# Performance work log

Measured on AMD Instinct MI355X. Metric: run time of the kernel, lower is better.

## Reference

```python
import jax, jax.numpy as jnp
import numpy as np

NUM_HEADS = 12
PER_HEAD_DIM = 64
EMBED_DIM = NUM_HEADS * PER_HEAD_DIM
MAX_LEN = 1024  # max_position_embeddings - 1


def setup_inputs() -> dict:
    key = jax.random.key(0)
    k1, k2, k3 = jax.random.split(key, 3)
    pre_proj_emb = jax.random.normal(k1, (8, MAX_LEN, EMBED_DIM), dtype=jnp.float32)
    # trunc_normal_(mean=0, std=1, a=0, b=1) ~ values in [0,1); uniform is a faithful stand-in for random init
    toeplitz_psfs = jax.random.uniform(k2, (NUM_HEADS, 2 * MAX_LEN - 1, PER_HEAD_DIM), dtype=jnp.float32)
    proj_w = jax.random.normal(k3, (EMBED_DIM, EMBED_DIM), dtype=jnp.float32) * (1.0 / np.sqrt(EMBED_DIM))
    proj_b = jnp.zeros((EMBED_DIM,), dtype=jnp.float32)
    return {"pre_proj_emb": pre_proj_emb, "toeplitz_psfs": toeplitz_psfs, "proj_w": proj_w, "proj_b": proj_b}


def reference(pre_proj_emb, toeplitz_psfs, proj_w, proj_b):
    B, L, D = pre_proj_emb.shape
    H, dh = NUM_HEADS, PER_HEAD_DIM
    # pad sequence to 2L-1 and split heads: [B, 2L-1, H, dh] -> [B, H, 2L-1, dh]
    padded = jnp.pad(pre_proj_emb, ((0, 0), (0, L - 1), (0, 0)))
    padded = padded.reshape(B, 2 * L - 1, H, dh).transpose(0, 2, 1, 3)
    # softmax over the 2L-1 filter taps, then causal mask (keep first L taps)
    psfs = jax.nn.softmax(toeplitz_psfs, axis=1)
    causal_mask = jnp.concatenate([jnp.ones((L,), jnp.float32), jnp.zeros((L - 1,), jnp.float32)])
    psfs = psfs * causal_mask[None, :, None]  # [H, 2L-1, dh]
    # 2D FFT over (taps, per-head-dim) axes, pointwise multiply, inverse, take real part
    psfs_fft = jnp.fft.fftn(psfs, axes=(1, 2))            # [H, 2L-1, dh]
    emb_fft = jnp.fft.fftn(padded, axes=(2, 3))           # [B, H, 2L-1, dh]
    conv = jnp.real(jnp.fft.ifftn(psfs_fft[None] * emb_fft, axes=(2, 3)))[:, :, :L, :]
    # exact (erf) gelu to match torch F.gelu default
    conv = jax.nn.gelu(conv, approximate=False)
    conv = conv.transpose(0, 2, 1, 3).reshape(B, L, H * dh)
    conv_emb = conv @ proj_w.T + proj_b
    return (conv_emb, psfs)
```

## Files before the change

kernel.cpp:

```cpp
#include <hip/hip_runtime.h>
#include <hip/hip_bf16.h>
#include <math.h>

#define NH 12
#define DH 64
#define SL 1024
#define NB 8
#define ED 768
#define NTAP 2047
#define NF 33
#define NSEQ 2048

typedef __attribute__((ext_vector_type(8))) short bf16x8;
typedef __attribute__((ext_vector_type(4))) float f32x4;
typedef __attribute__((ext_vector_type(4))) unsigned short ushort4v;

#define GLB_U32(p) ((const __attribute__((address_space(1))) unsigned int*)(p))
#define LDS_U32(p) ((__attribute__((address_space(3))) unsigned int*)(p))

__device__ __forceinline__ float2 cadd(float2 a, float2 b){ return make_float2(a.x+b.x, a.y+b.y); }
__device__ __forceinline__ float2 csub(float2 a, float2 b){ return make_float2(a.x-b.x, a.y-b.y); }
__device__ __forceinline__ float2 cmul(float2 a, float2 b){ return make_float2(a.x*b.x - a.y*b.y, a.x*b.y + a.y*b.x); }

__device__ __forceinline__ unsigned short bf16bits(float f) {
    __hip_bfloat16 hb = __float2bfloat16(f);
    return *reinterpret_cast<unsigned short*>(&hb);
}
__device__ __forceinline__ float bf16val(unsigned short u) {
    __hip_bfloat16 hb = *reinterpret_cast<__hip_bfloat16*>(&u);
    return __bfloat162float(hb);
}
__device__ __forceinline__ unsigned int pack2(float a, float b) {
    return (unsigned int)bf16bits(a) | ((unsigned int)bf16bits(b) << 16);
}

#define FPAD(i) ((i) + ((i) >> 3))

template<int DIR>
__device__ __forceinline__ void dft4v(float2 v[4]) {
    float2 e0 = cadd(v[0], v[2]), e1 = csub(v[0], v[2]);
    float2 o0 = cadd(v[1], v[3]), o1 = csub(v[1], v[3]);
    float2 o1t = (DIR < 0) ? make_float2(o1.y, -o1.x) : make_float2(-o1.y, o1.x);
    v[0] = cadd(e0, o0);
    v[1] = cadd(e1, o1t);
    v[2] = csub(e0, o0);
    v[3] = csub(e1, o1t);
}

template<int DIR>
__device__ __forceinline__ void dft8v(float2 v[8]) {
    const float RS = 0.70710678118654752440f;
    float2 e[4] = { v[0], v[2], v[4], v[6] };
    float2 o[4] = { v[1], v[3], v[5], v[7] };
    dft4v<DIR>(e);
    dft4v<DIR>(o);
    float2 t1 = (DIR < 0) ? make_float2(RS * (o[1].x + o[1].y), RS * (o[1].y - o[1].x))
                          : make_float2(RS * (o[1].x - o[1].y), RS * (o[1].y + o[1].x));
    float2 t2 = (DIR < 0) ? make_float2(o[2].y, -o[2].x) : make_float2(-o[2].y, o[2].x);
    float2 t3 = (DIR < 0) ? make_float2(RS * (o[3].y - o[3].x), RS * (-o[3].x - o[3].y))
                          : make_float2(RS * (-o[3].x - o[3].y), RS * (o[3].x - o[3].y));
    v[0] = cadd(e[0], o[0]); v[4] = csub(e[0], o[0]);
    v[1] = cadd(e[1], t1);   v[5] = csub(e[1], t1);
    v[2] = cadd(e[2], t2);   v[6] = csub(e[2], t2);
    v[3] = cadd(e[3], t3);   v[7] = csub(e[3], t3);
}

template<int DIR, int L, int R>
__device__ __forceinline__ void fft_stage(const float* __restrict__ sr, const float* __restrict__ si,
                                          float* __restrict__ dr, float* __restrict__ di,
                                          const float2* __restrict__ twd, int tid) {
    const int T = 2048 / R;
    #pragma unroll
    for (int jj = 0; jj < T; jj += 256) {
        int j = tid + jj;
        int k = j & (L - 1);
        int blk = j / L;
        float2 v[R];
        #pragma unroll
        for (int r = 0; r < R; ++r) {
            int idx = FPAD(j + T * r);
            v[r] = make_float2(sr[idx], si[idx]);
        }
        if (L > 1) {
            const int c = 2048 / (R * L);
            float2 w1 = twd[c * k];
            if (DIR > 0) w1.y = -w1.y;
            float2 w = w1;
            v[1] = cmul(v[1], w);
            #pragma unroll
            for (int r = 2; r < R; ++r) { w = cmul(w, w1); v[r] = cmul(v[r], w); }
        }
        if (R == 8) dft8v<DIR>(v); else dft4v<DIR>(v);
        int base = blk * (R * L) + k;
        #pragma unroll
        for (int r = 0; r < R; ++r) {
            int idx = FPAD(base + L * r);
            dr[idx] = v[r].x; di[idx] = v[r].y;
        }
    }
}

__device__ __forceinline__ void gen_twd(float2* twd, int tid) {
    for (int i = tid; i < 512; i += 256) {
        float ang = -6.28318530717958647692f * (float)i / 2048.0f;
        twd[i] = make_float2(cosf(ang), sinf(ang));
    }
}

__global__ void k1a_partial(const float* __restrict__ tp, const float* __restrict__ W,
                            float* __restrict__ pSum, float* __restrict__ psf_out,
                            ushort* __restrict__ Wh) {
    __shared__ float ls[4][64];
    int c = blockIdx.x, h = blockIdx.y;
    int tid = threadIdx.x, w = tid >> 6, e = tid & 63;
    const float* base = tp + (size_t)h * NTAP * 64;
    float* ob = psf_out + (size_t)h * NTAP * 64;
    float s = 0.f;
    #pragma unroll
    for (int i = 0; i < 16; ++i) {
        int row = c * 64 + w + 4 * i;
        if (row < NTAP) {
            float v = base[(size_t)row * 64 + e];
            s += expf(v - 1.0f);
            if (row >= SL) ob[(size_t)row * 64 + e] = 0.0f;
        }
    }
    ls[w][e] = s;
    __syncthreads();
    if (w == 0) {
        float S = s + ls[1][e] + ls[2][e] + ls[3][e];
        pSum[(h * 32 + c) * 64 + e] = S;
    }
    int bb = h * 32 + c;
    int base_w = bb * 1536;
    #pragma unroll
    for (int i = 0; i < 6; ++i) {
        int j = base_w + tid + i * 256;
        Wh[j] = bf16bits(W[j]);
    }
}

__global__ __launch_bounds__(256) void k2_mfma(const float* __restrict__ tp,
                                               const float* __restrict__ pSum,
                                               float* __restrict__ psf_out,
                                               float2* __restrict__ Pc) {
    __shared__ union {
        struct { ushort EH[128][72]; ushort CH[80][72]; } s;
        float Dl[66][133];
    } u;
    __shared__ float sInv[64];
    const int t0 = blockIdx.x * 128;
    const int h = blockIdx.y;
    const int tid = threadIdx.x, lane = tid & 63, w = tid >> 6;

    if (tid < 64) {
        float S = 0.f;
        #pragma unroll
        for (int cc = 0; cc < 32; ++cc) S += pSum[(h * 32 + cc) * 64 + tid];
        sInv[tid] = 1.0f / S;
    }
    __syncthreads();

    for (int i = tid; i < 128 * 16; i += 256) {
        int r = i >> 4, q = i & 15;
        float4 v = *(const float4*)&tp[((size_t)h * NTAP + t0 + r) * 64 + q * 4];
        float p0 = expf(v.x - 1.0f) * sInv[q * 4 + 0];
        float p1 = expf(v.y - 1.0f) * sInv[q * 4 + 1];
        float p2 = expf(v.z - 1.0f) * sInv[q * 4 + 2];
        float p3 = expf(v.w - 1.0f) * sInv[q * 4 + 3];
        *(float4*)&psf_out[((size_t)h * NTAP + t0 + r) * 64 + q * 4] = make_float4(p0, p1, p2, p3);
        *(unsigned int*)&u.s.EH[r][q * 4]     = pack2(p0, p1);
        *(unsigned int*)&u.s.EH[r][q * 4 + 2] = pack2(p2, p3);
    }
    for (int i = tid; i < 80 * 32; i += 256) {
        int c = i >> 5, e2 = (i & 31) * 2;
        float v0 = 0.f, v1 = 0.f;
        if (c < 33) {
            v0 = cosf(0.09817477042468103870f * (float)((c * e2) & 63));
            v1 = cosf(0.09817477042468103870f * (float)((c * (e2 + 1)) & 63));
        } else if (c < 66) {
            v0 = -sinf(0.09817477042468103870f * (float)(((c - 33) * e2) & 63));
            v1 = -sinf(0.09817477042468103870f * (float)(((c - 33) * (e2 + 1)) & 63));
        }
        *(unsigned int*)&u.s.CH[c][e2] = pack2(v0, v1);
    }
    __syncthreads();

    f32x4 acc[2][5] = {};
    const int lr = lane & 15, lg = lane >> 4;
    #pragma unroll
    for (int ks = 0; ks < 64; ks += 32) {
        const int kg = ks + lg * 8;
        bf16x8 bh8[5];
        #pragma unroll
        for (int n = 0; n < 5; ++n) bh8[n] = *(const bf16x8*)&u.s.CH[n * 16 + lr][kg];
        #pragma unroll
        for (int m = 0; m < 2; ++m) {
            bf16x8 ah8 = *(const bf16x8*)&u.s.EH[w * 32 + m * 16 + lr][kg];
            #pragma unroll
            for (int n = 0; n < 5; ++n)
                acc[m][n] = __builtin_amdgcn_mfma_f32_16x16x32_bf16(ah8, bh8[n], acc[m][n], 0, 0, 0);
        }
    }
    __syncthreads();
    #pragma unroll
    for (int n = 0; n < 5; ++n) {
        int c = n * 16 + lr;
        if (c < 66) {
            #pragma unroll
            for (int m = 0; m < 2; ++m)
                #pragma unroll
                for (int j = 0; j < 4; ++j)
                    u.Dl[c][w * 32 + m * 16 + lg * 4 + j] = acc[m][n][j];
        }
    }
    __syncthreads();
    for (int i = tid; i < 33 * 128; i += 256) {
        int f = i >> 7, t = i & 127;
        Pc[(size_t)(h * NF + f) * SL + t0 + t] = make_float2(u.Dl[f][t], u.Dl[f + 33][t]);
    }
}

__global__ __launch_bounds__(256) void k3_psf_fft(const float2* __restrict__ Pc, unsigned int* __restrict__ Pf) {
    __shared__ float Ar[2304], Ai[2304], Br[2304], Bi[2304];
    __shared__ float2 twd[512];
    int h = blockIdx.x / NF, f = blockIdx.x % NF;
    int tid = threadIdx.x;
    gen_twd(twd, tid);
    const float2* src = Pc + (size_t)(h * NF + f) * SL;
    {
        float2 v[8];
        #pragma unroll
        for (int r = 0; r < 4; ++r) v[r] = src[tid + 256 * r];
        #pragma unroll
        for (int r = 4; r < 8; ++r) v[r] = make_float2(0.f, 0.f);
        dft8v<-1>(v);
        #pragma unroll
        for (int r = 0; r < 8; ++r) {
            int idx = FPAD(tid * 8 + r);
            Ar[idx] = v[r].x; Ai[idx] = v[r].y;
        }
    }
    __syncthreads();
    fft_stage<-1, 8, 8>(Ar, Ai, Br, Bi, twd, tid);  __syncthreads();
    fft_stage<-1, 64, 8>(Br, Bi, Ar, Ai, twd, tid); __syncthreads();
    unsigned int* dst = Pf + (size_t)(h * NF + f) * NSEQ;
    #pragma unroll
    for (int jj = 0; jj < 512; jj += 256) {
        int j = tid + jj;
        float2 v[4];
        #pragma unroll
        for (int r = 0; r < 4; ++r) {
            int idx = FPAD(j + 512 * r);
            v[r] = make_float2(Ar[idx], Ai[idx]);
        }
        float2 w1 = twd[j];
        float2 w = w1;
        v[1] = cmul(v[1], w);
        w = cmul(w, w1); v[2] = cmul(v[2], w);
        w = cmul(w, w1); v[3] = cmul(v[3], w);
        dft4v<-1>(v);
        #pragma unroll
        for (int r = 0; r < 4; ++r) dst[j + 512 * r] = pack2(v[r].x, v[r].y);
    }
}

__global__ __launch_bounds__(256) void k4_mfma(const float* __restrict__ emb,
                                               ushort* __restrict__ XcRe, ushort* __restrict__ XcIm) {
    __shared__ union {
        struct { ushort EH[128][72]; ushort CH[80][72]; } s;
        float Dl[66][133];
    } u;
    const int t0 = blockIdx.x * 128;
    const int bh = blockIdx.y;
    const int b = bh / NH, h = bh % NH;
    const int tid = threadIdx.x, lane = tid & 63, w = tid >> 6;

    for (int i = tid; i < 128 * 16; i += 256) {
        int r = i >> 4, q = i & 15;
        float4 v = *(const float4*)&emb[((size_t)b * SL + t0 + r) * ED + h * 64 + q * 4];
        *(unsigned int*)&u.s.EH[r][q * 4]     = pack2(v.x, v.y);
        *(unsigned int*)&u.s.EH[r][q * 4 + 2] = pack2(v.z, v.w);
    }
    for (int i = tid; i < 80 * 32; i += 256) {
        int c = i >> 5, e2 = (i & 31) * 2;
        float v0 = 0.f, v1 = 0.f;
        if (c < 33) {
            v0 = cosf(0.09817477042468103870f * (float)((c * e2) & 63));
            v1 = cosf(0.09817477042468103870f * (float)((c * (e2 + 1)) & 63));
        } else if (c < 66) {
            v0 = -sinf(0.09817477042468103870f * (float)(((c - 33) * e2) & 63));
            v1 = -sinf(0.09817477042468103870f * (float)(((c - 33) * (e2 + 1)) & 63));
        }
        *(unsigned int*)&u.s.CH[c][e2] = pack2(v0, v1);
    }
    __syncthreads();

    f32x4 acc[2][5] = {};
    const int lr = lane & 15, lg = lane >> 4;
    #pragma unroll
    for (int ks = 0; ks < 64; ks += 32) {
        const int kg = ks + lg * 8;
        bf16x8 bh8[5];
        #pragma unroll
        for (int n = 0; n < 5; ++n) bh8[n] = *(const bf16x8*)&u.s.CH[n * 16 + lr][kg];
        #pragma unroll
        for (int m = 0; m < 2; ++m) {
            bf16x8 ah8 = *(const bf16x8*)&u.s.EH[w * 32 + m * 16 + lr][kg];
            #pragma unroll
            for (int n = 0; n < 5; ++n)
                acc[m][n] = __builtin_amdgcn_mfma_f32_16x16x32_bf16(ah8, bh8[n], acc[m][n], 0, 0, 0);
        }
    }
    __syncthreads();
    #pragma unroll
    for (int n = 0; n < 5; ++n) {
        int c = n * 16 + lr;
        if (c < 66) {
            #pragma unroll
            for (int m = 0; m < 2; ++m)
                #pragma unroll
                for (int j = 0; j < 4; ++j)
                    u.Dl[c][w * 32 + m * 16 + lg * 4 + j] = acc[m][n][j];
        }
    }
    __syncthreads();
    for (int i = tid; i < 66 * 128; i += 256) {
        int c = i >> 7, t = i & 127;
        unsigned short val = bf16bits(u.Dl[c][t]);
        if (c < 33) XcRe[(size_t)(bh * NF + c) * SL + t0 + t] = val;
        else        XcIm[(size_t)(bh * NF + (c - 33)) * SL + t0 + t] = val;
    }
}

__global__ __launch_bounds__(256) void k5_seq_conv(ushort* __restrict__ XcRe, ushort* __restrict__ XcIm,
                                                   const unsigned int* __restrict__ Pf) {
    __shared__ float Ar[2304], Ai[2304], Br[2304], Bi[2304];
    __shared__ float2 twd[512];
    int f = blockIdx.x % NF;
    int bh = blockIdx.x / NF;
    int h = bh % NH;
    int tid = threadIdx.x;
    gen_twd(twd, tid);
    ushort* xre = XcRe + (size_t)(bh * NF + f) * SL;
    ushort* xim = XcIm + (size_t)(bh * NF + f) * SL;
    {
        float2 v[8];
        #pragma unroll
        for (int r = 0; r < 4; ++r)
            v[r] = make_float2(bf16val(xre[tid + 256 * r]), bf16val(xim[tid + 256 * r]));
        #pragma unroll
        for (int r = 4; r < 8; ++r) v[r] = make_float2(0.f, 0.f);
        dft8v<-1>(v);
        #pragma unroll
        for (int r = 0; r < 8; ++r) {
            int idx = FPAD(tid * 8 + r);
            Ar[idx] = v[r].x; Ai[idx] = v[r].y;
        }
    }
    __syncthreads();
    fft_stage<-1, 8, 8>(Ar, Ai, Br, Bi, twd, tid);   __syncthreads();
    fft_stage<-1, 64, 8>(Br, Bi, Ar, Ai, twd, tid);  __syncthreads();
    {
        const unsigned int* pf = Pf + (size_t)(h * NF + f) * NSEQ;
        #pragma unroll
        for (int jj = 0; jj < 512; jj += 256) {
            int j = tid + jj;
            float2 v[4];
            #pragma unroll
            for (int r = 0; r < 4; ++r) {
                int idx = FPAD(j + 512 * r);
                v[r] = make_float2(Ar[idx], Ai[idx]);
            }
            float2 w1 = twd[j];
            float2 w = w1;
            v[1] = cmul(v[1], w);
            w = cmul(w, w1); v[2] = cmul(v[2], w);
            w = cmul(w, w1); v[3] = cmul(v[3], w);
            dft4v<-1>(v);
            #pragma unroll
            for (int r = 0; r < 4; ++r) {
                unsigned int p = pf[j + 512 * r];
                float2 pv = make_float2(bf16val((unsigned short)(p & 0xFFFF)),
                                        bf16val((unsigned short)(p >> 16)));
                float2 m = cmul(v[r], pv);
                int idx = FPAD(j + 512 * r);
                Br[idx] = m.x; Bi[idx] = m.y;
            }
        }
    }
    __syncthreads();
    fft_stage<1, 1, 8>(Br, Bi, Ar, Ai, twd, tid);  __syncthreads();
    fft_stage<1, 8, 8>(Ar, Ai, Br, Bi, twd, tid);  __syncthreads();
    fft_stage<1, 64, 8>(Br, Bi, Ar, Ai, twd, tid); __syncthreads();
    const float sc = 1.0f / 2048.0f;
    #pragma unroll
    for (int jj = 0; jj < 512; jj += 256) {
        int j = tid + jj;
        float2 v[4];
        #pragma unroll
        for (int r = 0; r < 4; ++r) {
            int idx = FPAD(j + 512 * r);
            v[r] = make_float2(Ar[idx], Ai[idx]);
        }
        float2 w1 = twd[j];
        w1.y = -w1.y;
        float2 w = w1;
        v[1] = cmul(v[1], w);
        w = cmul(w, w1); v[2] = cmul(v[2], w);
        w = cmul(w, w1); v[3] = cmul(v[3], w);
        dft4v<1>(v);
        xre[j] = bf16bits(v[0].x * sc);        xim[j] = bf16bits(v[0].y * sc);
        xre[j + 512] = bf16bits(v[1].x * sc);  xim[j + 512] = bf16bits(v[1].y * sc);
    }
}

__global__ __launch_bounds__(256) void k6_mfma(const ushort* __restrict__ XcRe,
                                               const ushort* __restrict__ XcIm,
                                               ushort* __restrict__ Gh) {
    __shared__ union {
        float Y32[64][133];
        ushort CH[64][72];
    } uy;
    __shared__ ushort YH[128][72];
    const int t0 = blockIdx.x * 128;
    const int bh = blockIdx.y;
    const int b = bh / NH, h = bh % NH;
    const int tid = threadIdx.x, lane = tid & 63, w = tid >> 6;

    for (int i = tid; i < 64 * 32; i += 256) {
        int c = i >> 5, tq = i & 31;
        const ushort* src = (c < 33) ? XcRe + (size_t)(bh * NF + c) * SL
                                     : XcIm + (size_t)(bh * NF + (c - 32)) * SL;
        ushort4v v = *(const ushort4v*)&src[t0 + tq * 4];
        uy.Y32[c][tq * 4 + 0] = bf16val(v.x); uy.Y32[c][tq * 4 + 1] = bf16val(v.y);
        uy.Y32[c][tq * 4 + 2] = bf16val(v.z); uy.Y32[c][tq * 4 + 3] = bf16val(v.w);
    }
    __syncthreads();
    for (int i = tid; i < 128 * 8; i += 256) {
        int t = i & 127, c0 = (i >> 7) * 8;
        float v[8];
        #pragma unroll
        for (int j = 0; j < 8; ++j) v[j] = uy.Y32[c0 + j][t];
        #pragma unroll
        for (int j = 0; j < 8; j += 2)
            *(unsigned int*)&YH[t][c0 + j] = pack2(v[j], v[j + 1]);
    }
    __syncthreads();
    for (int i = tid; i < 64 * 32; i += 256) {
        int e = i >> 5, c2 = (i & 31) * 2;
        float v[2];
        #pragma unroll
        for (int j = 0; j < 2; ++j) {
            int c = c2 + j;
            if (c <= 32) {
                float wt = (c == 0 || c == 32) ? (1.0f / 64.0f) : (2.0f / 64.0f);
                v[j] = wt * cosf(0.09817477042468103870f * (float)((c * e) & 63));
            } else {
                v[j] = -(2.0f / 64.0f) * sinf(0.09817477042468103870f * (float)(((c - 32) * e) & 63));
            }
        }
        *(unsigned int*)&uy.CH[e][c2] = pack2(v[0], v[1]);
    }
    __syncthreads();

    f32x4 acc[2][4] = {};
    const int lr = lane & 15, lg = lane >> 4;
    #pragma unroll
    for (int ks = 0; ks < 64; ks += 32) {
        const int kg = ks + lg * 8;
        bf16x8 bh8[4];
        #pragma unroll
        for (int n = 0; n < 4; ++n) bh8[n] = *(const bf16x8*)&uy.CH[n * 16 + lr][kg];
        #pragma unroll
        for (int m = 0; m < 2; ++m) {
            bf16x8 ah8 = *(const bf16x8*)&YH[w * 32 + m * 16 + lr][kg];
            #pragma unroll
            for (int n = 0; n < 4; ++n)
                acc[m][n] = __builtin_amdgcn_mfma_f32_16x16x32_bf16(ah8, bh8[n], acc[m][n], 0, 0, 0);
        }
    }
    #pragma unroll
    for (int n = 0; n < 4; ++n) {
        const int col = h * 64 + n * 16 + lr;
        #pragma unroll
        for (int m = 0; m < 2; ++m) {
            #pragma unroll
            for (int j = 0; j < 4; ++j) {
                int t = t0 + w * 32 + m * 16 + lg * 4 + j;
                float v = acc[m][n][j];
                float g = 0.5f * v * (1.0f + erff(v * 0.70710678118654752440f));
                Gh[((size_t)b * SL + t) * ED + col] = bf16bits(g);
            }
        }
    }
}

#define K7STAGE(p, kk) do { \
    const ushort* gA_ = Gh + (size_t)(i0 + aRow) * ED + (kk) + stCol; \
    const ushort* gB_ = Wh + (size_t)(j0 + bRow) * ED + (kk) + stCol; \
    __builtin_amdgcn_global_load_lds(GLB_U32(gA_),           LDS_U32(&Ah[p][aBase]),        16, 0, 0); \
    __builtin_amdgcn_global_load_lds(GLB_U32(gA_ + 8 * ED),  LDS_U32(&Ah[p][aBase + 512]),  16, 0, 0); \
    __builtin_amdgcn_global_load_lds(GLB_U32(gB_),           LDS_U32(&Bh[p][bBase]),        16, 0, 0); \
    __builtin_amdgcn_global_load_lds(GLB_U32(gB_ + 8 * ED),  LDS_U32(&Bh[p][bBase + 512]),  16, 0, 0); \
    __builtin_amdgcn_global_load_lds(GLB_U32(gB_ + 16 * ED), LDS_U32(&Bh[p][bBase + 1024]), 16, 0, 0); \
    __builtin_amdgcn_global_load_lds(GLB_U32(gB_ + 24 * ED), LDS_U32(&Bh[p][bBase + 1536]), 16, 0, 0); \
} while (0)

__global__ __launch_bounds__(256) void k7_mfma(
        const ushort* __restrict__ Gh, const ushort* __restrict__ Wh,
        const float* __restrict__ bias, float* __restrict__ out) {
    __shared__ ushort Ah[2][64 * 64];
    __shared__ ushort Bh[2][128 * 64];
    const int bid = blockIdx.y * gridDim.x + blockIdx.x;
    const int swz = (bid & 7) * 96 + (bid >> 3);
    const int j0 = (swz % 6) * 128;
    const int i0 = (swz / 6) * 64;
    const int tid = threadIdx.x;
    const int lane = tid & 63, wid = tid >> 6;
    const int wm = wid >> 1, wn = wid & 1;

    const int aRow = wid * 16 + (lane >> 3);
    const int bRow = wid * 32 + (lane >> 3);
    const int stCol = (((lane & 7) ^ ((lane >> 3) & 7)) * 8);
    const int aBase = wid * 1024;
    const int bBase = wid * 2048;

    f32x4 acc[2][4] = {};

    const int lr = lane & 15, lg = lane >> 4;
    const int arow = wm * 32 + lr;
    const int brow = wn * 64 + lr;
    const int sw0 = ((lg ^ (lr & 7)) * 8);
    const int sw1 = (((4 + lg) ^ (lr & 7)) * 8);

    K7STAGE(0, 0);

    for (int t = 0; t < 12; ++t) {
        const int cur = t & 1;
        if (t < 11) {
            K7STAGE(cur ^ 1, (t + 1) * 64);
            asm volatile("s_waitcnt vmcnt(6)" ::: "memory");
        } else {
            asm volatile("s_waitcnt vmcnt(0)" ::: "memory");
        }
        __builtin_amdgcn_s_barrier();

        #pragma unroll
        for (int ks = 0; ks < 2; ++ks) {
            const int sw = ks ? sw1 : sw0;
            bf16x8 a0 = *(const bf16x8*)&Ah[cur][arow * 64 + sw];
            bf16x8 a1 = *(const bf16x8*)&Ah[cur][(arow + 16) * 64 + sw];
            bf16x8 b0 = *(const bf16x8*)&Bh[cur][brow * 64 + sw];
            bf16x8 b1 = *(const bf16x8*)&Bh[cur][(brow + 16) * 64 + sw];
            bf16x8 b2 = *(const bf16x8*)&Bh[cur][(brow + 32) * 64 + sw];
            bf16x8 b3 = *(const bf16x8*)&Bh[cur][(brow + 48) * 64 + sw];
            acc[0][0] = __builtin_amdgcn_mfma_f32_16x16x32_bf16(a0, b0, acc[0][0], 0, 0, 0);
            acc[0][1] = __builtin_amdgcn_mfma_f32_16x16x32_bf16(a0, b1, acc[0][1], 0, 0, 0);
            acc[0][2] = __builtin_amdgcn_mfma_f32_16x16x32_bf16(a0, b2, acc[0][2], 0, 0, 0);
            acc[0][3] = __builtin_amdgcn_mfma_f32_16x16x32_bf16(a0, b3, acc[0][3], 0, 0, 0);
            acc[1][0] = __builtin_amdgcn_mfma_f32_16x16x32_bf16(a1, b0, acc[1][0], 0, 0, 0);
            acc[1][1] = __builtin_amdgcn_mfma_f32_16x16x32_bf16(a1, b1, acc[1][1], 0, 0, 0);
            acc[1][2] = __builtin_amdgcn_mfma_f32_16x16x32_bf16(a1, b2, acc[1][2], 0, 0, 0);
            acc[1][3] = __builtin_amdgcn_mfma_f32_16x16x32_bf16(a1, b3, acc[1][3], 0, 0, 0);
        }
        asm volatile("s_waitcnt lgkmcnt(0)" ::: "memory");
        __builtin_amdgcn_s_barrier();
    }

    const int ocol0 = j0 + wn * 64 + lr;
    const int orow0 = i0 + wm * 32 + (lane >> 4) * 4;
    #pragma unroll
    for (int n = 0; n < 4; ++n) {
        const float bv = bias[ocol0 + n * 16];
        #pragma unroll
        for (int m = 0; m < 2; ++m) {
            #pragma unroll
            for (int j = 0; j < 4; ++j) {
                out[(size_t)(orow0 + m * 16 + j) * ED + ocol0 + n * 16] = acc[m][n][j] + bv;
            }
        }
    }
}

extern "C" void kernel_launch(void* const* d_in, const int* in_sizes, int n_in,
                              void* d_out, int out_size, void* d_ws, size_t ws_size,
                              hipStream_t stream) {
    (void)in_sizes; (void)n_in; (void)out_size; (void)ws_size;
    const float* emb  = (const float*)d_in[0];
    const float* tp   = (const float*)d_in[1];
    const float* W    = (const float*)d_in[2];
    const float* bias = (const float*)d_in[3];

    float* out_conv = (float*)d_out;
    float* out_psf  = out_conv + (size_t)NB * SL * ED;

    float2*       Pc = (float2*)d_ws;
    unsigned int* Pf = (unsigned int*)(Pc + (size_t)NH * NF * SL);
    ushort* XcRe = (ushort*)(Pf + (size_t)NH * NF * NSEQ);
    ushort* XcIm = XcRe + (size_t)NB * NH * NF * SL;
    ushort* Gh   = XcIm + (size_t)NB * NH * NF * SL;
    ushort* Whh  = Gh + (size_t)NB * SL * ED;
    float* pSum = (float*)Pf;

    k1a_partial<<<dim3(32, NH), dim3(256), 0, stream>>>(tp, W, pSum, out_psf, Whh);
    k2_mfma<<<dim3(SL / 128, NH), dim3(256), 0, stream>>>(tp, pSum, out_psf, Pc);
    k3_psf_fft<<<dim3(NH * NF), dim3(256), 0, stream>>>(Pc, Pf);
    k4_mfma<<<dim3(SL / 128, NB * NH), dim3(256), 0, stream>>>(emb, XcRe, XcIm);
    k5_seq_conv<<<dim3(NB * NH * NF), dim3(256), 0, stream>>>(XcRe, XcIm, Pf);
    k6_mfma<<<dim3(SL / 128, NB * NH), dim3(256), 0, stream>>>(XcRe, XcIm, Gh);
    k7_mfma<<<dim3(ED / 128, (NB * SL) / 64), dim3(256), 0, stream>>>(
        Gh, Whh, bias, out_conv);
}
```

Baseline: 98.03 us.

## Merge softmax-partial and embedding DFT kernels, store FFT scratch as packed fp16

Folds the softmax partial-sum and weight conversion kernel into the embedding head-dim DFT kernel as extra blocks of one launch, removing a launch and letting the two independent jobs overlap. The psf DFT kernel is retiled to 64 rows per block to give it more blocks. Sequence FFT scratch in shared memory is stored as packed fp16 complex instead of separate fp32 arrays, halving LDS footprint and traffic to improve occupancy. The psf spectrum is also stored in fp16 rather than bf16. The fp16 intermediates risk range and precision loss in the FFT.

```diff
diff --git a/kernel.cpp b/kernel.cpp
--- a/kernel.cpp
+++ b/kernel.cpp
@@ -1,5 +1,6 @@
 #include <hip/hip_runtime.h>
 #include <hip/hip_bf16.h>
+#include <hip/hip_fp16.h>
 #include <math.h>
 
 #define NH 12
@@ -32,6 +33,20 @@
 }
 __device__ __forceinline__ unsigned int pack2(float a, float b) {
     return (unsigned int)bf16bits(a) | ((unsigned int)bf16bits(b) << 16);
+}
+__device__ __forceinline__ unsigned short h16(float f) {
+    __half h = __float2half_rn(f);
+    return *reinterpret_cast<unsigned short*>(&h);
+}
+__device__ __forceinline__ float h2f(unsigned short u) {
+    __half h = *reinterpret_cast<__half*>(&u);
+    return __half2float(h);
+}
+__device__ __forceinline__ unsigned int hpk(float2 v) {
+    return (unsigned int)h16(v.x) | ((unsigned int)h16(v.y) << 16);
+}
+__device__ __forceinline__ float2 hup(unsigned int u) {
+    return make_float2(h2f((unsigned short)(u & 0xFFFF)), h2f((unsigned short)(u >> 16)));
 }
 
 #define FPAD(i) ((i) + ((i) >> 3))
@@ -66,9 +81,9 @@
 }
 
 template<int DIR, int L, int R>
-__device__ __forceinline__ void fft_stage(const float* __restrict__ sr, const float* __restrict__ si,
-                                          float* __restrict__ dr, float* __restrict__ di,
-                                          const float2* __restrict__ twd, int tid) {
+__device__ __forceinline__ void fft_stage_h(const unsigned int* __restrict__ s,
+                                            unsigned int* __restrict__ d,
+                                            const float2* __restrict__ twd, int tid) {
     const int T = 2048 / R;
     #pragma unroll
     for (int jj = 0; jj < T; jj += 256) {
@@ -77,10 +92,7 @@
         int blk = j / L;
         float2 v[R];
         #pragma unroll
-        for (int r = 0; r < R; ++r) {
-            int idx = FPAD(j + T * r);
-            v[r] = make_float2(sr[idx], si[idx]);
-        }
+        for (int r = 0; r < R; ++r) v[r] = hup(s[FPAD(j + T * r)]);
         if (L > 1) {
             const int c = 2048 / (R * L);
             float2 w1 = twd[c * k];
@@ -93,10 +105,7 @@
         if (R == 8) dft8v<DIR>(v); else dft4v<DIR>(v);
         int base = blk * (R * L) + k;
         #pragma unroll
-        for (int r = 0; r < R; ++r) {
-            int idx = FPAD(base + L * r);
-            dr[idx] = v[r].x; di[idx] = v[r].y;
-        }
+        for (int r = 0; r < R; ++r) d[FPAD(base + L * r)] = hpk(v[r]);
     }
 }
 
@@ -107,36 +116,109 @@
     }
 }
 
-__global__ void k1a_partial(const float* __restrict__ tp, const float* __restrict__ W,
-                            float* __restrict__ pSum, float* __restrict__ psf_out,
-                            ushort* __restrict__ Wh) {
+__global__ __launch_bounds__(256) void k4_fat(const float* __restrict__ emb,
+                                              const float* __restrict__ tp,
+                                              const float* __restrict__ W,
+                                              float* __restrict__ pSum,
+                                              float* __restrict__ psf_out,
+                                              ushort* __restrict__ Wh,
+                                              ushort* __restrict__ XcRe, ushort* __restrict__ XcIm) {
+    __shared__ union {
+        struct { ushort EH[128][72]; ushort CH[80][72]; } s;
+        float Dl[66][133];
+    } u;
     __shared__ float ls[4][64];
-    int c = blockIdx.x, h = blockIdx.y;
-    int tid = threadIdx.x, w = tid >> 6, e = tid & 63;
-    const float* base = tp + (size_t)h * NTAP * 64;
-    float* ob = psf_out + (size_t)h * NTAP * 64;
-    float s = 0.f;
-    #pragma unroll
-    for (int i = 0; i < 16; ++i) {
-        int row = c * 64 + w + 4 * i;
-        if (row < NTAP) {
-            float v = base[(size_t)row * 64 + e];
-            s += expf(v - 1.0f);
-            if (row >= SL) ob[(size_t)row * 64 + e] = 0.0f;
-        }
-    }
-    ls[w][e] = s;
-    __syncthreads();
-    if (w == 0) {
-        float S = s + ls[1][e] + ls[2][e] + ls[3][e];
-        pSum[(h * 32 + c) * 64 + e] = S;
-    }
-    int bb = h * 32 + c;
-    int base_w = bb * 1536;
-    #pragma unroll
-    for (int i = 0; i < 6; ++i) {
-        int j = base_w + tid + i * 256;
-        Wh[j] = bf16bits(W[j]);
+    const int tid = threadIdx.x, lane = tid & 63, w = tid >> 6;
+
+    if (blockIdx.x >= 768) {
+        int idx = blockIdx.x - 768;
+        int c = idx & 31, h = idx >> 5;
+        const float* base = tp + (size_t)h * NTAP * 64;
+        float* ob = psf_out + (size_t)h * NTAP * 64;
+        int e = lane;
+        float s = 0.f;
+        #pragma unroll
+        for (int i = 0; i < 16; ++i) {
+            int row = c * 64 + w + 4 * i;
+            if (row < NTAP) {
+                float v = base[(size_t)row * 64 + e];
+                s += expf(v - 1.0f);
+                if (row >= SL) ob[(size_t)row * 64 + e] = 0.0f;
+            }
+        }
+        ls[w][e] = s;
+        __syncthreads();
+        if (w == 0) {
+            float S = s + ls[1][e] + ls[2][e] + ls[3][e];
+            pSum[(h * 32 + c) * 64 + e] = S;
+        }
+        int base_w = idx * 1536;
+        #pragma unroll
+        for (int i = 0; i < 6; ++i) {
+            int j = base_w + tid + i * 256;
+            Wh[j] = bf16bits(W[j]);
+        }
+        return;
+    }
+
+    const int t0 = (blockIdx.x & 7) * 128;
+    const int bh = blockIdx.x >> 3;
+    const int b = bh / NH, h = bh % NH;
+
+    for (int i = tid; i < 128 * 16; i += 256) {
+        int r = i >> 4, q = i & 15;
+        float4 v = *(const float4*)&emb[((size_t)b * SL + t0 + r) * ED + h * 64 + q * 4];
+        *(unsigned int*)&u.s.EH[r][q * 4]     = pack2(v.x, v.y);
+        *(unsigned int*)&u.s.EH[r][q * 4 + 2] = pack2(v.z, v.w);
+    }
+    for (int i = tid; i < 80 * 32; i += 256) {
+        int c = i >> 5, e2 = (i & 31) * 2;
+        float v0 = 0.f, v1 = 0.f;
+        if (c < 33) {
+            v0 = cosf(0.09817477042468103870f * (float)((c * e2) & 63));
+            v1 = cosf(0.09817477042468103870f * (float)((c * (e2 + 1)) & 63));
+        } else if (c < 66) {
+            v0 = -sinf(0.09817477042468103870f * (float)(((c - 33) * e2) & 63));
+            v1 = -sinf(0.09817477042468103870f * (float)(((c - 33) * (e2 + 1)) & 63));
+        }
+        *(unsigned int*)&u.s.CH[c][e2] = pack2(v0, v1);
+    }
+    __syncthreads();
+
+    f32x4 acc[2][5] = {};
+    const int lr = lane & 15, lg = lane >> 4;
+    #pragma unroll
+    for (int ks = 0; ks < 64; ks += 32) {
+        const int kg = ks + lg * 8;
+        bf16x8 bh8[5];
+        #pragma unroll
+        for (int n = 0; n < 5; ++n) bh8[n] = *(const bf16x8*)&u.s.CH[n * 16 + lr][kg];
+        #pragma unroll
+        for (int m = 0; m < 2; ++m) {
+            bf16x8 ah8 = *(const bf16x8*)&u.s.EH[w * 32 + m * 16 + lr][kg];
+            #pragma unroll
+            for (int n = 0; n < 5; ++n)
+                acc[m][n] = __builtin_amdgcn_mfma_f32_16x16x32_bf16(ah8, bh8[n], acc[m][n], 0, 0, 0);
+        }
+    }
+    __syncthreads();
+    #pragma unroll
+    for (int n = 0; n < 5; ++n) {
+        int c = n * 16 + lr;
+        if (c < 66) {
+            #pragma unroll
+            for (int m = 0; m < 2; ++m)
+                #pragma unroll
+                for (int j = 0; j < 4; ++j)
+                    u.Dl[c][w * 32 + m * 16 + lg * 4 + j] = acc[m][n][j];
+        }
+    }
+    __syncthreads();
+    for (int i = tid; i < 66 * 128; i += 256) {
+        int c = i >> 7, t = i & 127;
+        unsigned short val = bf16bits(u.Dl[c][t]);
+        if (c < 33) XcRe[(size_t)(bh * NF + c) * SL + t0 + t] = val;
+        else        XcIm[(size_t)(bh * NF + (c - 33)) * SL + t0 + t] = val;
     }
 }
 
@@ -145,11 +227,11 @@
                                                float* __restrict__ psf_out,
                                                float2* __restrict__ Pc) {
     __shared__ union {
-        struct { ushort EH[128][72]; ushort CH[80][72]; } s;
-        float Dl[66][133];
+        struct { ushort EH[64][72]; ushort CH[80][72]; } s;
+        float Dl[66][72];
     } u;
     __shared__ float sInv[64];
-    const int t0 = blockIdx.x * 128;
+    const int t0 = blockIdx.x * 64;
     const int h = blockIdx.y;
     const int tid = threadIdx.x, lane = tid & 63, w = tid >> 6;
 
@@ -161,7 +243,7 @@
     }
     __syncthreads();
 
-    for (int i = tid; i < 128 * 16; i += 256) {
+    for (int i = tid; i < 64 * 16; i += 256) {
         int r = i >> 4, q = i & 15;
         float4 v = *(const float4*)&tp[((size_t)h * NTAP + t0 + r) * 64 + q * 4];
         float p0 = expf(v.x - 1.0f) * sInv[q * 4 + 0];
@@ -186,7 +268,7 @@
     }
     __syncthreads();
 
-    f32x4 acc[2][5] = {};
+    f32x4 acc[5] = {};
     const int lr = lane & 15, lg = lane >> 4;
     #pragma unroll
     for (int ks = 0; ks < 64; ks += 32) {
@@ -194,13 +276,10 @@
         bf16x8 bh8[5];
         #pragma unroll
         for (int n = 0; n < 5; ++n) bh8[n] = *(const bf16x8*)&u.s.CH[n * 16 + lr][kg];
-        #pragma unroll
-        for (int m = 0; m < 2; ++m) {
-            bf16x8 ah8 = *(const bf16x8*)&u.s.EH[w * 32 + m * 16 + lr][kg];
-            #pragma unroll
-            for (int n = 0; n < 5; ++n)
-                acc[m][n] = __builtin_amdgcn_mfma_f32_16x16x32_bf16(ah8, bh8[n], acc[m][n], 0, 0, 0);
-        }
+        bf16x8 ah8 = *(const bf16x8*)&u.s.EH[w * 16 + lr][kg];
+        #pragma unroll
+        for (int n = 0; n < 5; ++n)
+            acc[n] = __builtin_amdgcn_mfma_f32_16x16x32_bf16(ah8, bh8[n], acc[n], 0, 0, 0);
     }
     __syncthreads();
     #pragma unroll
@@ -208,21 +287,19 @@
         int c = n * 16 + lr;
         if (c < 66) {
             #pragma unroll
-            for (int m = 0; m < 2; ++m)
-                #pragma unroll
-                for (int j = 0; j < 4; ++j)
-                    u.Dl[c][w * 32 + m * 16 + lg * 4 + j] = acc[m][n][j];
-        }
-    }
-    __syncthreads();
-    for (int i = tid; i < 33 * 128; i += 256) {
-        int f = i >> 7, t = i & 127;
+            for (int j = 0; j < 4; ++j)
+                u.Dl[c][w * 16 + lg * 4 + j] = acc[n][j];
+        }
+    }
+    __syncthreads();
+    for (int i = tid; i < 33 * 64; i += 256) {
+        int f = i >> 6, t = i & 63;
         Pc[(size_t)(h * NF + f) * SL + t0 + t] = make_float2(u.Dl[f][t], u.Dl[f + 33][t]);
     }
 }
 
 __global__ __launch_bounds__(256) void k3_psf_fft(const float2* __restrict__ Pc, unsigned int* __restrict__ Pf) {
-    __shared__ float Ar[2304], Ai[2304], Br[2304], Bi[2304];
+    __shared__ unsigned int A[2304], B[2304];
     __shared__ float2 twd[512];
     int h = blockIdx.x / NF, f = blockIdx.x % NF;
     int tid = threadIdx.x;
@@ -236,24 +313,18 @@
         for (int r = 4; r < 8; ++r) v[r] = make_float2(0.f, 0.f);
         dft8v<-1>(v);
         #pragma unroll
-        for (int r = 0; r < 8; ++r) {
-            int idx = FPAD(tid * 8 + r);
-            Ar[idx] = v[r].x; Ai[idx] = v[r].y;
-        }
-    }
-    __syncthreads();
-    fft_stage<-1, 8, 8>(Ar, Ai, Br, Bi, twd, tid);  __syncthreads();
-    fft_stage<-1, 64, 8>(Br, Bi, Ar, Ai, twd, tid); __syncthreads();
+        for (int r = 0; r < 8; ++r) A[FPAD(tid * 8 + r)] = hpk(v[r]);
+    }
+    __syncthreads();
+    fft_stage_h<-1, 8, 8>(A, B, twd, tid);  __syncthreads();
+    fft_stage_h<-1, 64, 8>(B, A, twd, tid); __syncthreads();
     unsigned int* dst = Pf + (size_t)(h * NF + f) * NSEQ;
     #pragma unroll
     for (int jj = 0; jj < 512; jj += 256) {
         int j = tid + jj;
         float2 v[4];
         #pragma unroll
-        for (int r = 0; r < 4; ++r) {
-            int idx = FPAD(j + 512 * r);
-            v[r] = make_float2(Ar[idx], Ai[idx]);
-        }
+        for (int r = 0; r < 4; ++r) v[r] = hup(A[FPAD(j + 512 * r)]);
         float2 w1 = twd[j];
         float2 w = w1;
         v[1] = cmul(v[1], w);
@@ -261,81 +332,13 @@
         w = cmul(w, w1); v[3] = cmul(v[3], w);
         dft4v<-1>(v);
         #pragma unroll
-        for (int r = 0; r < 4; ++r) dst[j + 512 * r] = pack2(v[r].x, v[r].y);
-    }
-}
-
-__global__ __launch_bounds__(256) void k4_mfma(const float* __restrict__ emb,
-                                               ushort* __restrict__ XcRe, ushort* __restrict__ XcIm) {
-    __shared__ union {
-        struct { ushort EH[128][72]; ushort CH[80][72]; } s;
-        float Dl[66][133];
-    } u;
-    const int t0 = blockIdx.x * 128;
-    const int bh = blockIdx.y;
-    const int b = bh / NH, h = bh % NH;
-    const int tid = threadIdx.x, lane = tid & 63, w = tid >> 6;
-
-    for (int i = tid; i < 128 * 16; i += 256) {
-        int r = i >> 4, q = i & 15;
-        float4 v = *(const float4*)&emb[((size_t)b * SL + t0 + r) * ED + h * 64 + q * 4];
-        *(unsigned int*)&u.s.EH[r][q * 4]     = pack2(v.x, v.y);
-        *(unsigned int*)&u.s.EH[r][q * 4 + 2] = pack2(v.z, v.w);
-    }
-    for (int i = tid; i < 80 * 32; i += 256) {
-        int c = i >> 5, e2 = (i & 31) * 2;
-        float v0 = 0.f, v1 = 0.f;
-        if (c < 33) {
-            v0 = cosf(0.09817477042468103870f * (float)((c * e2) & 63));
-            v1 = cosf(0.09817477042468103870f * (float)((c * (e2 + 1)) & 63));
-        } else if (c < 66) {
-            v0 = -sinf(0.09817477042468103870f * (float)(((c - 33) * e2) & 63));
-            v1 = -sinf(0.09817477042468103870f * (float)(((c - 33) * (e2 + 1)) & 63));
-        }
-        *(unsigned int*)&u.s.CH[c][e2] = pack2(v0, v1);
-    }
-    __syncthreads();
-
-    f32x4 acc[2][5] = {};
-    const int lr = lane & 15, lg = lane >> 4;
-    #pragma unroll
-    for (int ks = 0; ks < 64; ks += 32) {
-        const int kg = ks + lg * 8;
-        bf16x8 bh8[5];
-        #pragma unroll
-        for (int n = 0; n < 5; ++n) bh8[n] = *(const bf16x8*)&u.s.CH[n * 16 + lr][kg];
-        #pragma unroll
-        for (int m = 0; m < 2; ++m) {
-            bf16x8 ah8 = *(const bf16x8*)&u.s.EH[w * 32 + m * 16 + lr][kg];
-            #pragma unroll
-            for (int n = 0; n < 5; ++n)
-                acc[m][n] = __builtin_amdgcn_mfma_f32_16x16x32_bf16(ah8, bh8[n], acc[m][n], 0, 0, 0);
-        }
-    }
-    __syncthreads();
-    #pragma unroll
-    for (int n = 0; n < 5; ++n) {
-        int c = n * 16 + lr;
-        if (c < 66) {
-            #pragma unroll
-            for (int m = 0; m < 2; ++m)
-                #pragma unroll
-                for (int j = 0; j < 4; ++j)
-                    u.Dl[c][w * 32 + m * 16 + lg * 4 + j] = acc[m][n][j];
-        }
-    }
-    __syncthreads();
-    for (int i = tid; i < 66 * 128; i += 256) {
-        int c = i >> 7, t = i & 127;
-        unsigned short val = bf16bits(u.Dl[c][t]);
-        if (c < 33) XcRe[(size_t)(bh * NF + c) * SL + t0 + t] = val;
-        else        XcIm[(size_t)(bh * NF + (c - 33)) * SL + t0 + t] = val;
+        for (int r = 0; r < 4; ++r) dst[j + 512 * r] = hpk(v[r]);
     }
 }
 
 __global__ __launch_bounds__(256) void k5_seq_conv(ushort* __restrict__ XcRe, ushort* __restrict__ XcIm,
                                                    const unsigned int* __restrict__ Pf) {
-    __shared__ float Ar[2304], Ai[2304], Br[2304], Bi[2304];
+    __shared__ unsigned int A[2304], B[2304];
     __shared__ float2 twd[512];
     int f = blockIdx.x % NF;
     int bh = blockIdx.x / NF;
@@ -353,14 +356,11 @@
         for (int r = 4; r < 8; ++r) v[r] = make_float2(0.f, 0.f);
         dft8v<-1>(v);
         #pragma unroll
-        for (int r = 0; r < 8; ++r) {
-            int idx = FPAD(tid * 8 + r);
-            Ar[idx] = v[r].x; Ai[idx] = v[r].y;
-        }
-    }
-    __syncthreads();
-    fft_stage<-1, 8, 8>(Ar, Ai, Br, Bi, twd, tid);   __syncthreads();
-    fft_stage<-1, 64, 8>(Br, Bi, Ar, Ai, twd, tid);  __syncthreads();
+        for (int r = 0; r < 8; ++r) A[FPAD(tid * 8 + r)] = hpk(v[r]);
+    }
+    __syncthreads();
+    fft_stage_h<-1, 8, 8>(A, B, twd, tid);   __syncthreads();
+    fft_stage_h<-1, 64, 8>(B, A, twd, tid);  __syncthreads();
     {
         const unsigned int* pf = Pf + (size_t)(h * NF + f) * NSEQ;
         #pragma unroll
@@ -368,10 +368,7 @@
             int j = tid + jj;
             float2 v[4];
             #pragma unroll
-            for (int r = 0; r < 4; ++r) {
-                int idx = FPAD(j + 512 * r);
-                v[r] = make_float2(Ar[idx], Ai[idx]);
-            }
+            for (int r = 0; r < 4; ++r) v[r] = hup(A[FPAD(j + 512 * r)]);
             float2 w1 = twd[j];
             float2 w = w1;
             v[1] = cmul(v[1], w);
@@ -380,29 +377,22 @@
             dft4v<-1>(v);
             #pragma unroll
             for (int r = 0; r < 4; ++r) {
-                unsigned int p = pf[j + 512 * r];
-                float2 pv = make_float2(bf16val((unsigned short)(p & 0xFFFF)),
-                                        bf16val((unsigned short)(p >> 16)));
-                float2 m = cmul(v[r], pv);
-                int idx = FPAD(j + 512 * r);
-                Br[idx] = m.x; Bi[idx] = m.y;
+                float2 pv = hup(pf[j + 512 * r]);
+                B[FPAD(j + 512 * r)] = hpk(cmul(v[r], pv));
             }
         }
     }
     __syncthreads();
-    fft_stage<1, 1, 8>(Br, Bi, Ar, Ai, twd, tid);  __syncthreads();
-    fft_stage<1, 8, 8>(Ar, Ai, Br, Bi, twd, tid);  __syncthreads();
-    fft_stage<1, 64, 8>(Br, Bi, Ar, Ai, twd, tid); __syncthreads();
+    fft_stage_h<1, 1, 8>(B, A, twd, tid);  __syncthreads();
+    fft_stage_h<1, 8, 8>(A, B, twd, tid);  __syncthreads();
+    fft_stage_h<1, 64, 8>(B, A, twd, tid); __syncthreads();
     const float sc = 1.0f / 2048.0f;
     #pragma unroll
     for (int jj = 0; jj < 512; jj += 256) {
         int j = tid + jj;
         float2 v[4];
         #pragma unroll
-        for (int r = 0; r < 4; ++r) {
-            int idx = FPAD(j + 512 * r);
-            v[r] = make_float2(Ar[idx], Ai[idx]);
-        }
+        for (int r = 0; r < 4; ++r) v[r] = hup(A[FPAD(j + 512 * r)]);
         float2 w1 = twd[j];
         w1.y = -w1.y;
         float2 w = w1;
@@ -603,10 +593,9 @@
     ushort* Whh  = Gh + (size_t)NB * SL * ED;
     float* pSum = (float*)Pf;
 
-    k1a_partial<<<dim3(32, NH), dim3(256), 0, stream>>>(tp, W, pSum, out_psf, Whh);
-    k2_mfma<<<dim3(SL / 128, NH), dim3(256), 0, stream>>>(tp, pSum, out_psf, Pc);
+    k4_fat<<<dim3(1152), dim3(256), 0, stream>>>(emb, tp, W, pSum, out_psf, Whh, XcRe, XcIm);
+    k2_mfma<<<dim3(SL / 64, NH), dim3(256), 0, stream>>>(tp, pSum, out_psf, Pc);
     k3_psf_fft<<<dim3(NH * NF), dim3(256), 0, stream>>>(Pc, Pf);
-    k4_mfma<<<dim3(SL / 128, NB * NH), dim3(256), 0, stream>>>(emb, XcRe, XcIm);
     k5_seq_conv<<<dim3(NB * NH * NF), dim3(256), 0, stream>>>(XcRe, XcIm, Pf);
     k6_mfma<<<dim3(SL / 128, NB * NH), dim3(256), 0, stream>>>(XcRe, XcIm, Gh);
     k7_mfma<<<dim3(ED / 128, (NB * SL) / 64), dim3(256), 0, stream>>>(
```

Result: faster. 89.55 us, median of 2 (-8.7%).
